# Optimization experiments

Hardware: AMD Instinct MI355X
Metric: run time of the kernel (lower is better)

Reference implementation:

```python
import jax, jax.numpy as jnp
import numpy as np

NEG_SLOPE = 0.2  # PyG GATConv default


def gat_conv(x, src, dst, W, att_src, att_dst, bias, n_nodes):
    # x: [N, F_in]; W: [F_in, H*C]; att_*: [H, C]; bias: [H*C]
    H, C = att_src.shape
    h = (x @ W).reshape(n_nodes, H, C)                      # [N, H, C]
    a_src = jnp.sum(h * att_src, axis=-1)                   # [N, H]
    a_dst = jnp.sum(h * att_dst, axis=-1)                   # [N, H]
    e = jax.nn.leaky_relu(a_src[src] + a_dst[dst], NEG_SLOPE)  # [E, H]
    # segment softmax over incoming edges of each dst node
    e_max = jax.ops.segment_max(e, dst, num_segments=n_nodes)
    e_max = jnp.where(jnp.isfinite(e_max), e_max, 0.0)
    ex = jnp.exp(e - e_max[dst])                             # [E, H]
    denom = jax.ops.segment_sum(ex, dst, num_segments=n_nodes)
    alpha = ex / (denom[dst] + 1e-16)                        # [E, H]
    msg = h[src] * alpha[:, :, None]                         # [E, H, C]
    out = jax.ops.segment_sum(msg, dst, num_segments=n_nodes)  # [N, H, C]
    return out.reshape(n_nodes, H * C) + bias


def setup_inputs() -> dict:
    key = jax.random.key(0)
    ks = jax.random.split(key, 12)
    N, F_in, Hd, heads, F_out, E = 50000, 128, 32, 8, 16, 800000
    x = jax.random.normal(ks[0], (N, F_in), dtype=jnp.float32)
    edge_index = jax.random.randint(ks[1], (2, E), 0, N, dtype=jnp.int64)
    g = 0.1
    return {
        "x": x,
        "edge_index": edge_index,
        "W1": jax.random.normal(ks[2], (F_in, heads * Hd), dtype=jnp.float32) * g,
        "att_src1": jax.random.normal(ks[3], (heads, Hd), dtype=jnp.float32) * g,
        "att_dst1": jax.random.normal(ks[4], (heads, Hd), dtype=jnp.float32) * g,
        "b1": jnp.zeros((heads * Hd,), dtype=jnp.float32),
        "W2": jax.random.normal(ks[5], (heads * Hd, Hd), dtype=jnp.float32) * g,
        "att_src2": jax.random.normal(ks[6], (1, Hd), dtype=jnp.float32) * g,
        "att_dst2": jax.random.normal(ks[7], (1, Hd), dtype=jnp.float32) * g,
        "b2": jnp.zeros((Hd,), dtype=jnp.float32),
        "Wout": jax.random.normal(ks[8], (Hd, F_out), dtype=jnp.float32) * g,
        "bout": jnp.zeros((F_out,), dtype=jnp.float32),
    }


def reference(x, edge_index, W1, att_src1, att_dst1, b1, W2, att_src2, att_dst2, b2, Wout, bout):
    N = x.shape[0]
    # PyG GATConv adds self loops by default
    loops = jnp.arange(N, dtype=edge_index.dtype)
    src = jnp.concatenate([edge_index[0], loops])
    dst = jnp.concatenate([edge_index[1], loops])
    h = jax.nn.elu(gat_conv(x, src, dst, W1, att_src1, att_dst1, b1, N))
    # dropout is identity in eval mode
    h = jax.nn.elu(gat_conv(h, src, dst, W2, att_src2, att_dst2, b2, N))
    return h @ Wout + bout
```

## Files before the change

kernel.cpp:

```cpp
#include <hip/hip_runtime.h>
#include <math.h>

#define NEG_SLOPE 0.2f

__device__ __forceinline__ float bflo(unsigned int u) {
  union { unsigned int i; float f; } c;
  c.i = u << 16;
  return c.f;
}
__device__ __forceinline__ float bfhi(unsigned int u) {
  union { unsigned int i; float f; } c;
  c.i = u & 0xFFFF0000u;
  return c.f;
}
__device__ __forceinline__ unsigned short f2bf(float f) {
  union { float f; unsigned int i; } c;
  c.f = f;
  unsigned int i = c.i;
  return (unsigned short)((i + 0x7FFFu + ((i >> 16) & 1u)) >> 16);
}


__global__ __launch_bounds__(256) void hist_kernel(const int* __restrict__ ei,
                                                   int* __restrict__ counts, int e) {
  int i = blockIdx.x * 256 + threadIdx.x;
  if (i < e) atomicAdd(&counts[ei[e + i]], 1);
}

#define SCAN_TILE 2048
__global__ __launch_bounds__(256) void scan1_kernel(const int* __restrict__ counts,
                                                    int* __restrict__ offsets,
                                                    int* __restrict__ bsum, int n) {
  __shared__ int wtot[4];
  int tid = threadIdx.x;
  int base = blockIdx.x * SCAN_TILE + tid * 8;
  int v[8];
#pragma unroll
  for (int k = 0; k < 8; ++k) v[k] = (base + k < n) ? counts[base + k] + 1 : 0;
#pragma unroll
  for (int k = 1; k < 8; ++k) v[k] += v[k - 1];
  int tsum = v[7];
  int lane = tid & 63;
  int w = tid >> 6;
  int ws = tsum;
#pragma unroll
  for (int off = 1; off < 64; off <<= 1) {
    int t = __shfl_up(ws, off, 64);
    if (lane >= off) ws += t;
  }
  if (lane == 63) wtot[w] = ws;
  __syncthreads();
  int woff = 0;
#pragma unroll
  for (int k = 0; k < 3; ++k)
    if (k < w) woff += wtot[k];
  int thrBase = woff + ws - tsum;
#pragma unroll
  for (int k = 0; k < 8; ++k)
    if (base + k < n) offsets[base + k] = thrBase + v[k];
  if (tid == 255) bsum[blockIdx.x] = woff + ws;
}

__global__ __launch_bounds__(256) void scan3_kernel(const int* __restrict__ counts,
                                                    int* __restrict__ offsets,
                                                    const int* __restrict__ bsum,
                                                    int* __restrict__ cursor,
                                                    int n, int nb) {
  __shared__ int pres[64];
  int tid = threadIdx.x;
  if (tid < 64) {
    int v = (tid < nb) ? bsum[tid] : 0;
#pragma unroll
    for (int off = 1; off < 64; off <<= 1) {
      int t = __shfl_up(v, off, 64);
      if ((tid & 63) >= off) v += t;
    }
    pres[tid] = v;
  }
  __syncthreads();
  int i = blockIdx.x * 256 + tid;
  if (i > n) return;
  if (i == n) {
    offsets[n] = pres[nb - 1];
    return;
  }
  int b = i >> 11;
  int pre = (b == 0) ? 0 : pres[b - 1];
  int excl = pre + offsets[i] - (counts[i] + 1);
  offsets[i] = excl;
  cursor[i] = excl;
}

__global__ __launch_bounds__(256) void fill_kernel(const int* __restrict__ ei,
                                                   int* __restrict__ cursor,
                                                   int* __restrict__ csr, int n, int e) {
  int i = blockIdx.x * 256 + threadIdx.x;
  if (i < e) {
    int s = ei[i];
    int d = ei[e + i];
    int pos = atomicAdd(&cursor[d], 1);
    csr[pos] = s;
  } else if (i < e + n) {
    int node = i - e;
    int pos = atomicAdd(&cursor[node], 1);
    csr[pos] = node;
  } else if (i < e + n + 64) {
    csr[i] = 0;
  }
}


__global__ __launch_bounds__(256) void gemm1_kernel(const float* __restrict__ x,
                                                    const float* __restrict__ W1,
                                                    const float* __restrict__ att_src,
                                                    const float* __restrict__ att_dst,
                                                    unsigned short* __restrict__ h1b,
                                                    float* __restrict__ as1,
                                                    float* __restrict__ ad1, int n) {
  __shared__ float xst[32][132];
  __shared__ float wsm[32][128];
  int tid = threadIdx.x;
  int row0 = blockIdx.x * 128;
  int col0 = blockIdx.y * 128;
  int r0 = (tid >> 4) * 8, c0 = (tid & 15) * 8;
  float acc[8][8] = {};
  for (int k0 = 0; k0 < 128; k0 += 32) {
#pragma unroll
    for (int i = 0; i < 4; ++i) {
      int flat = tid + i * 256;
      int r = flat >> 3, c4 = flat & 7;
      float4 v = make_float4(0.f, 0.f, 0.f, 0.f);
      int gr = row0 + r;
      if (gr < n) v = *(const float4*)(x + (size_t)gr * 128 + k0 + c4 * 4);
      xst[c4 * 4 + 0][r] = v.x;
      xst[c4 * 4 + 1][r] = v.y;
      xst[c4 * 4 + 2][r] = v.z;
      xst[c4 * 4 + 3][r] = v.w;
    }
#pragma unroll
    for (int i = 0; i < 4; ++i) {
      int flat = tid + i * 256;
      int k = flat >> 5, c4 = flat & 31;
      *(float4*)&wsm[k][c4 * 4] = *(const float4*)(W1 + (size_t)(k0 + k) * 256 + col0 + c4 * 4);
    }
    __syncthreads();
    for (int k = 0; k < 32; ++k) {
      float4 xv0 = *(const float4*)&xst[k][r0];
      float4 xv1 = *(const float4*)&xst[k][r0 + 4];
      float4 wv0 = *(const float4*)&wsm[k][c0];
      float4 wv1 = *(const float4*)&wsm[k][c0 + 4];
      float xa[8] = {xv0.x, xv0.y, xv0.z, xv0.w, xv1.x, xv1.y, xv1.z, xv1.w};
      float wa[8] = {wv0.x, wv0.y, wv0.z, wv0.w, wv1.x, wv1.y, wv1.z, wv1.w};
#pragma unroll
      for (int i2 = 0; i2 < 8; ++i2)
#pragma unroll
        for (int j = 0; j < 8; ++j) acc[i2][j] += xa[i2] * wa[j];
    }
    __syncthreads();
  }
#pragma unroll
  for (int i2 = 0; i2 < 8; ++i2) {
    int gr = row0 + r0 + i2;
    if (gr < n) {
      unsigned int q[4];
#pragma unroll
      for (int j = 0; j < 4; ++j) {
        unsigned int lo = f2bf(acc[i2][j * 2]);
        unsigned int hi = f2bf(acc[i2][j * 2 + 1]);
        q[j] = lo | (hi << 16);
      }
      *(uint4*)(h1b + (size_t)gr * 256 + col0 + c0) = make_uint4(q[0], q[1], q[2], q[3]);
    }
  }
  int headG = blockIdx.y * 4 + ((tid & 15) >> 2);
  int cb = (tid & 3) * 8;
  float av[8], dv[8];
#pragma unroll
  for (int j = 0; j < 8; ++j) {
    av[j] = att_src[headG * 32 + cb + j];
    dv[j] = att_dst[headG * 32 + cb + j];
  }
#pragma unroll
  for (int i2 = 0; i2 < 8; ++i2) {
    float s1 = 0.f, s2 = 0.f;
#pragma unroll
    for (int j = 0; j < 8; ++j) {
      s1 += acc[i2][j] * av[j];
      s2 += acc[i2][j] * dv[j];
    }
    s1 += __shfl_xor(s1, 1);
    s1 += __shfl_xor(s1, 2);
    s2 += __shfl_xor(s2, 1);
    s2 += __shfl_xor(s2, 2);
    int gr = row0 + r0 + i2;
    if ((tid & 3) == 0 && gr < n) {
      as1[(size_t)gr * 8 + headG] = s1;
      ad1[(size_t)gr * 8 + headG] = s2;
    }
  }
}


__global__ __launch_bounds__(256) void agg1_kernel(const unsigned short* __restrict__ h1b,
                                                   const float* __restrict__ as1,
                                                   const float* __restrict__ ad1,
                                                   const int* __restrict__ offsets,
                                                   const int* __restrict__ csr,
                                                   const float* __restrict__ bias,
                                                   unsigned short* __restrict__ h1ob, int n) {
  __shared__ float peLds[4 * 64 * 8];
  int gtid = blockIdx.x * 256 + threadIdx.x;
  int node = gtid >> 6;
  int lane = gtid & 63;
  if (node >= n) return;
  float* myPe = peLds + (threadIdx.x >> 6) * 512;
  int beg = offsets[node], end = offsets[node + 1];
  int deg = end - beg;
  int half = lane >> 5, sub = lane & 31, head = sub >> 2;

  float4 adv0 = ((const float4*)(ad1 + (size_t)node * 8))[0];
  float4 adv1 = ((const float4*)(ad1 + (size_t)node * 8))[1];
  float ad_[8] = {adv0.x, adv0.y, adv0.z, adv0.w, adv1.x, adv1.y, adv1.z, adv1.w};

  float l = 0.f;
  float a[8] = {};

  for (int c0 = 0; c0 < deg; c0 += 64) {
    int cnt = min(64, deg - c0);
    bool valid = (c0 + lane) < deg;
    int s = csr[beg + c0 + lane];
    {
      const float4* ap = (const float4*)(as1 + (size_t)s * 8);
      float4 r0 = ap[0], r1 = ap[1];
      float asv[8] = {r0.x, r0.y, r0.z, r0.w, r1.x, r1.y, r1.z, r1.w};
      float4 q0, q1;
      float pv[8];
#pragma unroll
      for (int h = 0; h < 8; ++h) {
        float ev = asv[h] + ad_[h];
        ev = ev > 0.f ? ev : NEG_SLOPE * ev;
        pv[h] = valid ? __expf(ev) : 0.f;
      }
      q0 = make_float4(pv[0], pv[1], pv[2], pv[3]);
      q1 = make_float4(pv[4], pv[5], pv[6], pv[7]);
      *(float4*)&myPe[lane * 8 + 0] = q0;
      *(float4*)&myPe[lane * 8 + 4] = q1;
    }
#pragma unroll 2
    for (int j = 0; j < cnt; j += 2) {
      int e = j + half;
      int s2 = csr[beg + c0 + e];
      float pe = myPe[e * 8 + head];
      l += pe;
      uint4 hv = *(const uint4*)(h1b + (size_t)s2 * 256 + sub * 8);
      a[0] += pe * bflo(hv.x);
      a[1] += pe * bfhi(hv.x);
      a[2] += pe * bflo(hv.y);
      a[3] += pe * bfhi(hv.y);
      a[4] += pe * bflo(hv.z);
      a[5] += pe * bfhi(hv.z);
      a[6] += pe * bflo(hv.w);
      a[7] += pe * bfhi(hv.w);
    }
  }
  l += __shfl_xor(l, 32);
#pragma unroll
  for (int i = 0; i < 8; ++i) a[i] += __shfl_xor(a[i], 32);

  if (half == 0) {
    float inv = 1.f / (l + 1e-16f);
    const float4* bp = (const float4*)(bias + sub * 8);
    float4 b0 = bp[0], b1 = bp[1];
    float o[8];
    o[0] = a[0] * inv + b0.x;
    o[1] = a[1] * inv + b0.y;
    o[2] = a[2] * inv + b0.z;
    o[3] = a[3] * inv + b0.w;
    o[4] = a[4] * inv + b1.x;
    o[5] = a[5] * inv + b1.y;
    o[6] = a[6] * inv + b1.z;
    o[7] = a[7] * inv + b1.w;
    unsigned int q[4];
#pragma unroll
    for (int j = 0; j < 4; ++j) {
      float e0 = o[j * 2], e1 = o[j * 2 + 1];
      e0 = e0 > 0.f ? e0 : expm1f(e0);
      e1 = e1 > 0.f ? e1 : expm1f(e1);
      q[j] = (unsigned int)f2bf(e0) | ((unsigned int)f2bf(e1) << 16);
    }
    *(uint4*)(h1ob + (size_t)node * 256 + sub * 8) = make_uint4(q[0], q[1], q[2], q[3]);
  }
}


__global__ __launch_bounds__(256) void gemm2_kernel(const unsigned short* __restrict__ h1ob,
                                                    const float* __restrict__ W2,
                                                    const float* __restrict__ att_src,
                                                    const float* __restrict__ att_dst,
                                                    unsigned short* __restrict__ h2b,
                                                    float* __restrict__ as2,
                                                    float* __restrict__ ad2, int n) {
  __shared__ float xst[64][132];
  __shared__ float w2s[64][32];
  int tid = threadIdx.x;
  int row0 = blockIdx.x * 128;
  int r0 = (tid >> 3) * 4, c0 = (tid & 7) * 4;
  float acc[4][4] = {};
  for (int k0 = 0; k0 < 256; k0 += 64) {
#pragma unroll
    for (int i = 0; i < 4; ++i) {
      int flat = tid + i * 256;
      int r = flat >> 3, c8 = flat & 7;
      uint4 v = make_uint4(0, 0, 0, 0);
      int gr = row0 + r;
      if (gr < n) v = *(const uint4*)(h1ob + (size_t)gr * 256 + k0 + c8 * 8);
      int kb = c8 * 8;
      xst[kb + 0][r] = bflo(v.x);
      xst[kb + 1][r] = bfhi(v.x);
      xst[kb + 2][r] = bflo(v.y);
      xst[kb + 3][r] = bfhi(v.y);
      xst[kb + 4][r] = bflo(v.z);
      xst[kb + 5][r] = bfhi(v.z);
      xst[kb + 6][r] = bflo(v.w);
      xst[kb + 7][r] = bfhi(v.w);
    }
#pragma unroll
    for (int i = 0; i < 2; ++i) {
      int flat = tid + i * 256;
      int k = flat >> 3, c4 = flat & 7;
      *(float4*)&w2s[k][c4 * 4] = *(const float4*)(W2 + (size_t)(k0 + k) * 32 + c4 * 4);
    }
    __syncthreads();
    for (int k = 0; k < 64; ++k) {
      float4 xv = *(const float4*)&xst[k][r0];
      float4 wv = *(const float4*)&w2s[k][c0];
      float xa[4] = {xv.x, xv.y, xv.z, xv.w};
      float wa[4] = {wv.x, wv.y, wv.z, wv.w};
#pragma unroll
      for (int i2 = 0; i2 < 4; ++i2)
#pragma unroll
        for (int j = 0; j < 4; ++j) acc[i2][j] += xa[i2] * wa[j];
    }
    __syncthreads();
  }
#pragma unroll
  for (int i2 = 0; i2 < 4; ++i2) {
    int gr = row0 + r0 + i2;
    if (gr < n) {
      unsigned int q0 = (unsigned int)f2bf(acc[i2][0]) | ((unsigned int)f2bf(acc[i2][1]) << 16);
      unsigned int q1 = (unsigned int)f2bf(acc[i2][2]) | ((unsigned int)f2bf(acc[i2][3]) << 16);
      *(uint2*)(h2b + (size_t)gr * 32 + c0) = make_uint2(q0, q1);
    }
  }
  float av[4], dv[4];
#pragma unroll
  for (int j = 0; j < 4; ++j) {
    av[j] = att_src[c0 + j];
    dv[j] = att_dst[c0 + j];
  }
#pragma unroll
  for (int i2 = 0; i2 < 4; ++i2) {
    float s1 = 0.f, s2 = 0.f;
#pragma unroll
    for (int j = 0; j < 4; ++j) {
      s1 += acc[i2][j] * av[j];
      s2 += acc[i2][j] * dv[j];
    }
    s1 += __shfl_xor(s1, 1);
    s1 += __shfl_xor(s1, 2);
    s1 += __shfl_xor(s1, 4);
    s2 += __shfl_xor(s2, 1);
    s2 += __shfl_xor(s2, 2);
    s2 += __shfl_xor(s2, 4);
    int gr = row0 + r0 + i2;
    if ((tid & 7) == 0 && gr < n) {
      as2[gr] = s1;
      ad2[gr] = s2;
    }
  }
}


__global__ __launch_bounds__(256) void agg2_kernel(const unsigned short* __restrict__ h2b,
                                                   const float* __restrict__ as2,
                                                   const float* __restrict__ ad2,
                                                   const int* __restrict__ offsets,
                                                   const int* __restrict__ csr,
                                                   const float* __restrict__ bias,
                                                   const float* __restrict__ Wout,
                                                   const float* __restrict__ bout,
                                                   float* __restrict__ out, int n) {
  __shared__ float peLds[4 * 64];
  __shared__ float wLds[512];
  __shared__ float hrow[4][32];
  int tid = threadIdx.x;
  wLds[tid] = Wout[tid];
  wLds[tid + 256] = Wout[tid + 256];
  __syncthreads();

  int gtid = blockIdx.x * 256 + tid;
  int node = gtid >> 6;
  int lane = gtid & 63;
  if (node >= n) return;
  int wv = tid >> 6;
  float* myPe = peLds + wv * 64;
  float ad = ad2[node];
  int beg = offsets[node], end = offsets[node + 1];
  int deg = end - beg;
  int quarter = lane >> 4;
  int dsub = lane & 15;

  float l = 0.f, a0 = 0.f, a1 = 0.f;
  for (int c0 = 0; c0 < deg; c0 += 64) {
    int cnt = min(64, deg - c0);
    bool valid = (c0 + lane) < deg;
    int s = csr[beg + c0 + lane];
    float ev = as2[s] + ad;
    ev = ev > 0.f ? ev : NEG_SLOPE * ev;
    myPe[lane] = valid ? __expf(ev) : 0.f;
#pragma unroll 2
    for (int j = 0; j < cnt; j += 4) {
      int e = j + quarter;
      int s2 = csr[beg + c0 + e];
      float pe = myPe[e];
      l += pe;
      unsigned int hv = *(const unsigned int*)(h2b + (size_t)s2 * 32 + dsub * 2);
      a0 += pe * bflo(hv);
      a1 += pe * bfhi(hv);
    }
  }
  l += __shfl_xor(l, 16);
  l += __shfl_xor(l, 32);
  a0 += __shfl_xor(a0, 16);
  a1 += __shfl_xor(a1, 16);
  a0 += __shfl_xor(a0, 32);
  a1 += __shfl_xor(a1, 32);
  if (lane < 16) {
    float inv = 1.f / (l + 1e-16f);
    float o0 = a0 * inv + bias[dsub * 2];
    float o1 = a1 * inv + bias[dsub * 2 + 1];
    o0 = o0 > 0.f ? o0 : expm1f(o0);
    o1 = o1 > 0.f ? o1 : expm1f(o1);
    hrow[wv][dsub * 2] = o0;
    hrow[wv][dsub * 2 + 1] = o1;
  }
  if (lane < 16) {
    float s = bout[lane];
#pragma unroll
    for (int c = 0; c < 32; ++c) s += hrow[wv][c] * wLds[c * 16 + lane];
    out[(size_t)node * 16 + lane] = s;
  }
}


extern "C" void kernel_launch(void* const* d_in, const int* in_sizes, int n_in,
                              void* d_out, int out_size, void* d_ws, size_t ws_size,
                              hipStream_t stream) {
  const float* x        = (const float*)d_in[0];
  const int*   ei       = (const int*)d_in[1];
  const float* W1       = (const float*)d_in[2];
  const float* att_src1 = (const float*)d_in[3];
  const float* att_dst1 = (const float*)d_in[4];
  const float* b1       = (const float*)d_in[5];
  const float* W2       = (const float*)d_in[6];
  const float* att_src2 = (const float*)d_in[7];
  const float* att_dst2 = (const float*)d_in[8];
  const float* b2       = (const float*)d_in[9];
  const float* Wout     = (const float*)d_in[10];
  const float* bout     = (const float*)d_in[11];
  float* out = (float*)d_out;

  int n = in_sizes[0] / 128;
  int e = in_sizes[1] / 2;

  char* w = (char*)d_ws;
  unsigned short* h1b  = (unsigned short*)w; w += (size_t)n * 256 * 2;
  unsigned short* h1ob = (unsigned short*)w; w += (size_t)n * 256 * 2;
  unsigned short* h2b  = (unsigned short*)w; w += (size_t)n * 32 * 2;
  float* as1  = (float*)w; w += (size_t)n * 8 * 4;
  float* ad1  = (float*)w; w += (size_t)n * 8 * 4;
  float* as2  = (float*)w; w += (size_t)n * 4;
  float* ad2  = (float*)w; w += (size_t)n * 4;
  int* counts  = (int*)w; w += (size_t)n * 4;
  int* offsets = (int*)w; w += (size_t)(n + 16) * 4;
  int* cursor  = (int*)w; w += (size_t)n * 4;
  int* csr     = (int*)w; w += (size_t)(e + n + 64) * 4;
  int* bsum    = (int*)w; w += (size_t)256 * 4;

  int nb = (n + SCAN_TILE - 1) / SCAN_TILE;

  hipMemsetAsync(counts, 0, (size_t)n * 4, stream);
  hist_kernel<<<(e + 255) / 256, 256, 0, stream>>>(ei, counts, e);
  scan1_kernel<<<nb, 256, 0, stream>>>(counts, offsets, bsum, n);
  scan3_kernel<<<(n + 256) / 256, 256, 0, stream>>>(counts, offsets, bsum, cursor, n, nb);
  fill_kernel<<<(e + n + 64 + 255) / 256, 256, 0, stream>>>(ei, cursor, csr, n, e);

  gemm1_kernel<<<dim3((n + 127) / 128, 2), 256, 0, stream>>>(x, W1, att_src1, att_dst1,
                                                             h1b, as1, ad1, n);
  agg1_kernel<<<(n + 3) / 4, 256, 0, stream>>>(h1b, as1, ad1, offsets, csr, b1, h1ob, n);

  gemm2_kernel<<<(n + 127) / 128, 256, 0, stream>>>(h1ob, W2, att_src2, att_dst2,
                                                    h2b, as2, ad2, n);
  agg2_kernel<<<(n + 3) / 4, 256, 0, stream>>>(h2b, as2, ad2, offsets, csr, b2,
                                               Wout, bout, out, n);
}
```

Before: 366.7 us.

## Use bf16 MFMA for both GEMMs with pre-cast inputs and transposed weights

Replaces the FP32 LDS-tiled SIMT GEMMs in both GAT layers with bf16 MFMA 16x16x32 instructions. x is cast to bf16 and W1/W2 are cast and transposed by new pre-pass kernels so operands load directly as fragments. This targets the FP32 FMA cost of the projections. In exchange it adds two extra kernels and an extra read and write of x, reduces input precision to bf16, and replaces vectorized output stores with scalar 16-bit stores.

Result: faster. 342.7 us (-6.5%).

```diff
diff --git a/kernel.cpp b/kernel.cpp
--- a/kernel.cpp
+++ b/kernel.cpp
@@ -2,6 +2,9 @@
 #include <math.h>
 
 #define NEG_SLOPE 0.2f
+
+typedef __attribute__((ext_vector_type(8))) short bfrag8;
+typedef __attribute__((ext_vector_type(4))) float f4acc;
 
 __device__ __forceinline__ float bflo(unsigned int u) {
   union { unsigned int i; float f; } c;
@@ -110,92 +113,113 @@
 }
 
 
-__global__ __launch_bounds__(256) void gemm1_kernel(const float* __restrict__ x,
-                                                    const float* __restrict__ W1,
+__global__ __launch_bounds__(256) void wcast_kernel(const float* __restrict__ W1,
+                                                    const float* __restrict__ W2,
+                                                    unsigned short* __restrict__ w1t,
+                                                    unsigned short* __restrict__ w2t) {
+  int gid = blockIdx.x * 256 + threadIdx.x;
+#pragma unroll
+  for (int u = 0; u < 4; ++u) {
+    int j = gid * 4 + u;
+    if (j < 128 * 256) {
+      int k = j >> 8, c = j & 255;
+      w1t[c * 128 + k] = f2bf(W1[j]);
+    } else if (j < 128 * 256 + 256 * 32) {
+      int j2 = j - 128 * 256;
+      int k = j2 >> 5, c = j2 & 31;
+      w2t[c * 256 + k] = f2bf(W2[j2]);
+    }
+  }
+}
+
+__global__ __launch_bounds__(256) void xcast_kernel(const float* __restrict__ x,
+                                                    unsigned short* __restrict__ xb,
+                                                    int total) {
+  int gid = blockIdx.x * 256 + threadIdx.x;
+  int i = gid * 8;
+  if (i >= total) return;
+  float4 v0 = *(const float4*)(x + i);
+  float4 v1 = *(const float4*)(x + i + 4);
+  uint4 q;
+  q.x = (unsigned int)f2bf(v0.x) | ((unsigned int)f2bf(v0.y) << 16);
+  q.y = (unsigned int)f2bf(v0.z) | ((unsigned int)f2bf(v0.w) << 16);
+  q.z = (unsigned int)f2bf(v1.x) | ((unsigned int)f2bf(v1.y) << 16);
+  q.w = (unsigned int)f2bf(v1.z) | ((unsigned int)f2bf(v1.w) << 16);
+  *(uint4*)(xb + i) = q;
+}
+
+
+__global__ __launch_bounds__(256) void gemm1_kernel(const unsigned short* __restrict__ xb,
+                                                    const unsigned short* __restrict__ w1t,
                                                     const float* __restrict__ att_src,
                                                     const float* __restrict__ att_dst,
                                                     unsigned short* __restrict__ h1b,
                                                     float* __restrict__ as1,
                                                     float* __restrict__ ad1, int n) {
-  __shared__ float xst[32][132];
-  __shared__ float wsm[32][128];
   int tid = threadIdx.x;
-  int row0 = blockIdx.x * 128;
+  int wave = tid >> 6, lane = tid & 63;
+  int quad = lane >> 4, l16 = lane & 15;
+  int row0 = blockIdx.x * 64 + wave * 16;
   int col0 = blockIdx.y * 128;
-  int r0 = (tid >> 4) * 8, c0 = (tid & 15) * 8;
-  float acc[8][8] = {};
-  for (int k0 = 0; k0 < 128; k0 += 32) {
-#pragma unroll
-    for (int i = 0; i < 4; ++i) {
-      int flat = tid + i * 256;
-      int r = flat >> 3, c4 = flat & 7;
-      float4 v = make_float4(0.f, 0.f, 0.f, 0.f);
-      int gr = row0 + r;
-      if (gr < n) v = *(const float4*)(x + (size_t)gr * 128 + k0 + c4 * 4);
-      xst[c4 * 4 + 0][r] = v.x;
-      xst[c4 * 4 + 1][r] = v.y;
-      xst[c4 * 4 + 2][r] = v.z;
-      xst[c4 * 4 + 3][r] = v.w;
-    }
-#pragma unroll
-    for (int i = 0; i < 4; ++i) {
-      int flat = tid + i * 256;
-      int k = flat >> 5, c4 = flat & 31;
-      *(float4*)&wsm[k][c4 * 4] = *(const float4*)(W1 + (size_t)(k0 + k) * 256 + col0 + c4 * 4);
-    }
-    __syncthreads();
-    for (int k = 0; k < 32; ++k) {
-      float4 xv0 = *(const float4*)&xst[k][r0];
-      float4 xv1 = *(const float4*)&xst[k][r0 + 4];
-      float4 wv0 = *(const float4*)&wsm[k][c0];
-      float4 wv1 = *(const float4*)&wsm[k][c0 + 4];
-      float xa[8] = {xv0.x, xv0.y, xv0.z, xv0.w, xv1.x, xv1.y, xv1.z, xv1.w};
-      float wa[8] = {wv0.x, wv0.y, wv0.z, wv0.w, wv1.x, wv1.y, wv1.z, wv1.w};
-#pragma unroll
-      for (int i2 = 0; i2 < 8; ++i2)
-#pragma unroll
-        for (int j = 0; j < 8; ++j) acc[i2][j] += xa[i2] * wa[j];
-    }
-    __syncthreads();
-  }
-#pragma unroll
-  for (int i2 = 0; i2 < 8; ++i2) {
-    int gr = row0 + r0 + i2;
+  int rowA = min(row0 + l16, n - 1);
+
+  f4acc acc[8];
+#pragma unroll
+  for (int t = 0; t < 8; ++t) acc[t] = (f4acc)(0.f);
+
+#pragma unroll
+  for (int kc = 0; kc < 4; ++kc) {
+    bfrag8 a = *(const bfrag8*)(xb + (size_t)rowA * 128 + kc * 32 + quad * 8);
+#pragma unroll
+    for (int t = 0; t < 8; ++t) {
+      bfrag8 b = *(const bfrag8*)(w1t + (size_t)(col0 + t * 16 + l16) * 128 + kc * 32 + quad * 8);
+      acc[t] = __builtin_amdgcn_mfma_f32_16x16x32_bf16(a, b, acc[t], 0, 0, 0);
+    }
+  }
+
+#pragma unroll
+  for (int r = 0; r < 4; ++r) {
+    int gr = row0 + quad * 4 + r;
     if (gr < n) {
-      unsigned int q[4];
-#pragma unroll
-      for (int j = 0; j < 4; ++j) {
-        unsigned int lo = f2bf(acc[i2][j * 2]);
-        unsigned int hi = f2bf(acc[i2][j * 2 + 1]);
-        q[j] = lo | (hi << 16);
+#pragma unroll
+      for (int t = 0; t < 8; ++t)
+        h1b[(size_t)gr * 256 + col0 + t * 16 + l16] = f2bf(acc[t][r]);
+    }
+  }
+
+  float s1[4][4], s2[4][4];
+#pragma unroll
+  for (int r = 0; r < 4; ++r)
+#pragma unroll
+    for (int hl = 0; hl < 4; ++hl) { s1[r][hl] = 0.f; s2[r][hl] = 0.f; }
+#pragma unroll
+  for (int t = 0; t < 8; ++t) {
+    float av = att_src[col0 + t * 16 + l16];
+    float dv = att_dst[col0 + t * 16 + l16];
+    int hl = t >> 1;
+#pragma unroll
+    for (int r = 0; r < 4; ++r) {
+      s1[r][hl] += acc[t][r] * av;
+      s2[r][hl] += acc[t][r] * dv;
+    }
+  }
+#pragma unroll
+  for (int r = 0; r < 4; ++r) {
+#pragma unroll
+    for (int hl = 0; hl < 4; ++hl) {
+      float v1 = s1[r][hl], v2 = s2[r][hl];
+      v1 += __shfl_xor(v1, 1); v1 += __shfl_xor(v1, 2);
+      v1 += __shfl_xor(v1, 4); v1 += __shfl_xor(v1, 8);
+      v2 += __shfl_xor(v2, 1); v2 += __shfl_xor(v2, 2);
+      v2 += __shfl_xor(v2, 4); v2 += __shfl_xor(v2, 8);
+      if (l16 == 0) {
+        int gr = row0 + quad * 4 + r;
+        if (gr < n) {
+          int hg = (col0 >> 5) + hl;
+          as1[(size_t)gr * 8 + hg] = v1;
+          ad1[(size_t)gr * 8 + hg] = v2;
+        }
       }
-      *(uint4*)(h1b + (size_t)gr * 256 + col0 + c0) = make_uint4(q[0], q[1], q[2], q[3]);
-    }
-  }
-  int headG = blockIdx.y * 4 + ((tid & 15) >> 2);
-  int cb = (tid & 3) * 8;
-  float av[8], dv[8];
-#pragma unroll
-  for (int j = 0; j < 8; ++j) {
-    av[j] = att_src[headG * 32 + cb + j];
-    dv[j] = att_dst[headG * 32 + cb + j];
-  }
-#pragma unroll
-  for (int i2 = 0; i2 < 8; ++i2) {
-    float s1 = 0.f, s2 = 0.f;
-#pragma unroll
-    for (int j = 0; j < 8; ++j) {
-      s1 += acc[i2][j] * av[j];
-      s2 += acc[i2][j] * dv[j];
-    }
-    s1 += __shfl_xor(s1, 1);
-    s1 += __shfl_xor(s1, 2);
-    s2 += __shfl_xor(s2, 1);
-    s2 += __shfl_xor(s2, 2);
-    int gr = row0 + r0 + i2;
-    if ((tid & 3) == 0 && gr < n) {
-      as1[(size_t)gr * 8 + headG] = s1;
-      ad1[(size_t)gr * 8 + headG] = s2;
     }
   }
 }
@@ -233,7 +257,6 @@
       const float4* ap = (const float4*)(as1 + (size_t)s * 8);
       float4 r0 = ap[0], r1 = ap[1];
       float asv[8] = {r0.x, r0.y, r0.z, r0.w, r1.x, r1.y, r1.z, r1.w};
-      float4 q0, q1;
       float pv[8];
 #pragma unroll
       for (int h = 0; h < 8; ++h) {
@@ -241,10 +264,8 @@
         ev = ev > 0.f ? ev : NEG_SLOPE * ev;
         pv[h] = valid ? __expf(ev) : 0.f;
       }
-      q0 = make_float4(pv[0], pv[1], pv[2], pv[3]);
-      q1 = make_float4(pv[4], pv[5], pv[6], pv[7]);
-      *(float4*)&myPe[lane * 8 + 0] = q0;
-      *(float4*)&myPe[lane * 8 + 4] = q1;
+      *(float4*)&myPe[lane * 8 + 0] = make_float4(pv[0], pv[1], pv[2], pv[3]);
+      *(float4*)&myPe[lane * 8 + 4] = make_float4(pv[4], pv[5], pv[6], pv[7]);
     }
 #pragma unroll 2
     for (int j = 0; j < cnt; j += 2) {
@@ -294,88 +315,67 @@
 
 
 __global__ __launch_bounds__(256) void gemm2_kernel(const unsigned short* __restrict__ h1ob,
-                                                    const float* __restrict__ W2,
+                                                    const unsigned short* __restrict__ w2t,
                                                     const float* __restrict__ att_src,
                                                     const float* __restrict__ att_dst,
                                                     unsigned short* __restrict__ h2b,
                                                     float* __restrict__ as2,
                                                     float* __restrict__ ad2, int n) {
-  __shared__ float xst[64][132];
-  __shared__ float w2s[64][32];
   int tid = threadIdx.x;
-  int row0 = blockIdx.x * 128;
-  int r0 = (tid >> 3) * 4, c0 = (tid & 7) * 4;
-  float acc[4][4] = {};
-  for (int k0 = 0; k0 < 256; k0 += 64) {
-#pragma unroll
-    for (int i = 0; i < 4; ++i) {
-      int flat = tid + i * 256;
-      int r = flat >> 3, c8 = flat & 7;
-      uint4 v = make_uint4(0, 0, 0, 0);
-      int gr = row0 + r;
-      if (gr < n) v = *(const uint4*)(h1ob + (size_t)gr * 256 + k0 + c8 * 8);
-      int kb = c8 * 8;
-      xst[kb + 0][r] = bflo(v.x);
-      xst[kb + 1][r] = bfhi(v.x);
-      xst[kb + 2][r] = bflo(v.y);
-      xst[kb + 3][r] = bfhi(v.y);
-      xst[kb + 4][r] = bflo(v.z);
-      xst[kb + 5][r] = bfhi(v.z);
-      xst[kb + 6][r] = bflo(v.w);
-      xst[kb + 7][r] = bfhi(v.w);
-    }
-#pragma unroll
-    for (int i = 0; i < 2; ++i) {
-      int flat = tid + i * 256;
-      int k = flat >> 3, c4 = flat & 7;
-      *(float4*)&w2s[k][c4 * 4] = *(const float4*)(W2 + (size_t)(k0 + k) * 32 + c4 * 4);
-    }
-    __syncthreads();
-    for (int k = 0; k < 64; ++k) {
-      float4 xv = *(const float4*)&xst[k][r0];
-      float4 wv = *(const float4*)&w2s[k][c0];
-      float xa[4] = {xv.x, xv.y, xv.z, xv.w};
-      float wa[4] = {wv.x, wv.y, wv.z, wv.w};
-#pragma unroll
-      for (int i2 = 0; i2 < 4; ++i2)
-#pragma unroll
-        for (int j = 0; j < 4; ++j) acc[i2][j] += xa[i2] * wa[j];
-    }
-    __syncthreads();
-  }
-#pragma unroll
-  for (int i2 = 0; i2 < 4; ++i2) {
-    int gr = row0 + r0 + i2;
+  int wave = tid >> 6, lane = tid & 63;
+  int quad = lane >> 4, l16 = lane & 15;
+  int row0 = blockIdx.x * 64 + wave * 16;
+  int rowA = min(row0 + l16, n - 1);
+
+  f4acc acc[2];
+  acc[0] = (f4acc)(0.f);
+  acc[1] = (f4acc)(0.f);
+
+#pragma unroll
+  for (int kc = 0; kc < 8; ++kc) {
+    bfrag8 a = *(const bfrag8*)(h1ob + (size_t)rowA * 256 + kc * 32 + quad * 8);
+#pragma unroll
+    for (int t = 0; t < 2; ++t) {
+      bfrag8 b = *(const bfrag8*)(w2t + (size_t)(t * 16 + l16) * 256 + kc * 32 + quad * 8);
+      acc[t] = __builtin_amdgcn_mfma_f32_16x16x32_bf16(a, b, acc[t], 0, 0, 0);
+    }
+  }
+
+#pragma unroll
+  for (int r = 0; r < 4; ++r) {
+    int gr = row0 + quad * 4 + r;
     if (gr < n) {
-      unsigned int q0 = (unsigned int)f2bf(acc[i2][0]) | ((unsigned int)f2bf(acc[i2][1]) << 16);
-      unsigned int q1 = (unsigned int)f2bf(acc[i2][2]) | ((unsigned int)f2bf(acc[i2][3]) << 16);
-      *(uint2*)(h2b + (size_t)gr * 32 + c0) = make_uint2(q0, q1);
-    }
-  }
-  float av[4], dv[4];
-#pragma unroll
-  for (int j = 0; j < 4; ++j) {
-    av[j] = att_src[c0 + j];
-    dv[j] = att_dst[c0 + j];
-  }
-#pragma unroll
-  for (int i2 = 0; i2 < 4; ++i2) {
-    float s1 = 0.f, s2 = 0.f;
-#pragma unroll
-    for (int j = 0; j < 4; ++j) {
-      s1 += acc[i2][j] * av[j];
-      s2 += acc[i2][j] * dv[j];
-    }
-    s1 += __shfl_xor(s1, 1);
-    s1 += __shfl_xor(s1, 2);
-    s1 += __shfl_xor(s1, 4);
-    s2 += __shfl_xor(s2, 1);
-    s2 += __shfl_xor(s2, 2);
-    s2 += __shfl_xor(s2, 4);
-    int gr = row0 + r0 + i2;
-    if ((tid & 7) == 0 && gr < n) {
-      as2[gr] = s1;
-      ad2[gr] = s2;
+      h2b[(size_t)gr * 32 + l16] = f2bf(acc[0][r]);
+      h2b[(size_t)gr * 32 + 16 + l16] = f2bf(acc[1][r]);
+    }
+  }
+
+  float s1[4], s2v[4];
+#pragma unroll
+  for (int r = 0; r < 4; ++r) { s1[r] = 0.f; s2v[r] = 0.f; }
+#pragma unroll
+  for (int t = 0; t < 2; ++t) {
+    float av = att_src[t * 16 + l16];
+    float dv = att_dst[t * 16 + l16];
+#pragma unroll
+    for (int r = 0; r < 4; ++r) {
+      s1[r] += acc[t][r] * av;
+      s2v[r] += acc[t][r] * dv;
+    }
+  }
+#pragma unroll
+  for (int r = 0; r < 4; ++r) {
+    float v1 = s1[r], v2 = s2v[r];
+    v1 += __shfl_xor(v1, 1); v1 += __shfl_xor(v1, 2);
+    v1 += __shfl_xor(v1, 4); v1 += __shfl_xor(v1, 8);
+    v2 += __shfl_xor(v2, 1); v2 += __shfl_xor(v2, 2);
+    v2 += __shfl_xor(v2, 4); v2 += __shfl_xor(v2, 8);
+    if (l16 == 0) {
+      int gr = row0 + quad * 4 + r;
+      if (gr < n) {
+        as2[gr] = v1;
+        ad2[gr] = v2;
+      }
     }
   }
 }
@@ -476,7 +476,10 @@
   char* w = (char*)d_ws;
   unsigned short* h1b  = (unsigned short*)w; w += (size_t)n * 256 * 2;
   unsigned short* h1ob = (unsigned short*)w; w += (size_t)n * 256 * 2;
+  unsigned short* xb   = (unsigned short*)w; w += (size_t)n * 128 * 2;
   unsigned short* h2b  = (unsigned short*)w; w += (size_t)n * 32 * 2;
+  unsigned short* w1t  = (unsigned short*)w; w += (size_t)256 * 128 * 2;
+  unsigned short* w2t  = (unsigned short*)w; w += (size_t)32 * 256 * 2;
   float* as1  = (float*)w; w += (size_t)n * 8 * 4;
   float* ad1  = (float*)w; w += (size_t)n * 8 * 4;
   float* as2  = (float*)w; w += (size_t)n * 4;
@@ -495,12 +498,15 @@
   scan3_kernel<<<(n + 256) / 256, 256, 0, stream>>>(counts, offsets, bsum, cursor, n, nb);
   fill_kernel<<<(e + n + 64 + 255) / 256, 256, 0, stream>>>(ei, cursor, csr, n, e);
 
-  gemm1_kernel<<<dim3((n + 127) / 128, 2), 256, 0, stream>>>(x, W1, att_src1, att_dst1,
-                                                             h1b, as1, ad1, n);
+  wcast_kernel<<<40, 256, 0, stream>>>(W1, W2, w1t, w2t);
+  xcast_kernel<<<(n * 128 / 8 + 255) / 256, 256, 0, stream>>>(x, xb, n * 128);
+
+  gemm1_kernel<<<dim3((n + 63) / 64, 2), 256, 0, stream>>>(xb, w1t, att_src1, att_dst1,
+                                                           h1b, as1, ad1, n);
   agg1_kernel<<<(n + 3) / 4, 256, 0, stream>>>(h1b, as1, ad1, offsets, csr, b1, h1ob, n);
 
-  gemm2_kernel<<<(n + 127) / 128, 256, 0, stream>>>(h1ob, W2, att_src2, att_dst2,
-                                                    h2b, as2, ad2, n);
+  gemm2_kernel<<<(n + 63) / 64, 256, 0, stream>>>(h1ob, w2t, att_src2, att_dst2,
+                                                  h2b, as2, ad2, n);
   agg2_kernel<<<(n + 3) / 4, 256, 0, stream>>>(h2b, as2, ad2, offsets, csr, b2,
                                                Wout, bout, out, n);
 }
```
